# Optimization experiments

Measured on AMD Instinct MI355X. Metric: run time of the kernel, lower is better.

## Reference

```python
import jax, jax.numpy as jnp
import numpy as np

EPS = 1e-5
NUM_HEADS = 8


def setup_inputs() -> dict:
    key = jax.random.key(0)
    ks = jax.random.split(key, 6)
    B, C, S = 4, 512, 2048
    std = 0.02
    return {
        "hidden_states": jax.random.normal(ks[0], (B, C, S), dtype=jnp.float32),
        "gn_weight": jnp.ones((C,), dtype=jnp.float32),
        "gn_bias": jnp.zeros((C,), dtype=jnp.float32),
        "wq": jax.random.normal(ks[1], (C, C), dtype=jnp.float32) * std,
        "bq": jnp.zeros((C,), dtype=jnp.float32),
        "wk": jax.random.normal(ks[2], (C, C), dtype=jnp.float32) * std,
        "bk": jnp.zeros((C,), dtype=jnp.float32),
        "wv": jax.random.normal(ks[3], (C, C), dtype=jnp.float32) * std,
        "bv": jnp.zeros((C,), dtype=jnp.float32),
        "wo": jax.random.normal(ks[4], (C, C), dtype=jnp.float32) * std,
        "bo": jnp.zeros((C,), dtype=jnp.float32),
    }


def reference(hidden_states, gn_weight, gn_bias, wq, bq, wk, bk, wv, bv, wo, bo):
    # hidden_states: [B, C, S]
    x = hidden_states
    B, C, S = x.shape
    H = NUM_HEADS
    D = C // H

    # GroupNorm with 1 group: normalize over (C, S) per sample
    mean = jnp.mean(x, axis=(1, 2), keepdims=True)
    var = jnp.var(x, axis=(1, 2), keepdims=True)
    h = (x - mean) * jax.lax.rsqrt(var + EPS)
    h = h * gn_weight[None, :, None] + gn_bias[None, :, None]

    h = jnp.swapaxes(h, 1, 2)  # [B, S, C]

    q = h @ wq.T + bq  # [B, S, C]
    k = h @ wk.T + bk
    v = h @ wv.T + bv

    # split heads: [B, H, S, D]
    q = q.reshape(B, S, H, D).transpose(0, 2, 1, 3)
    k = k.reshape(B, S, H, D).transpose(0, 2, 1, 3)
    v = v.reshape(B, S, H, D).transpose(0, 2, 1, 3)

    scale = 1.0 / (D ** 0.25)  # applied to both q and k, as in source
    scores = jnp.einsum('bhqd,bhkd->bhqk', q * scale, k * scale)
    probs = jax.nn.softmax(scores, axis=-1)
    out = jnp.einsum('bhqk,bhkd->bhqd', probs, v)  # [B, H, S, D]

    out = out.transpose(0, 2, 1, 3).reshape(B, S, C)  # [B, S, C]
    out = out @ wo.T + bo
    out = jnp.swapaxes(out, 1, 2)  # [B, C, S]
    return out + hidden_states
```

## Files before the change

kernel.cpp:

```cpp
#include <hip/hip_runtime.h>

typedef __attribute__((ext_vector_type(8))) __bf16 bf16x8;
typedef __attribute__((ext_vector_type(4))) __bf16 bf16x4;
typedef __attribute__((ext_vector_type(4))) float f32x4;
typedef __attribute__((ext_vector_type(16))) float f32x16;

#define BSZ 4
#define CCH 512
#define SEQ 2048
#define NH  8
#define HD  64

__device__ __forceinline__ f32x4 mfma16(bf16x8 a, bf16x8 b, f32x4 c) {
  return __builtin_amdgcn_mfma_f32_16x16x32_bf16(a, b, c, 0, 0, 0);
}
__device__ __forceinline__ f32x16 mfma32(bf16x8 a, bf16x8 b, f32x16 c) {
  return __builtin_amdgcn_mfma_f32_32x32x16_bf16(a, b, c, 0, 0, 0);
}

__device__ __forceinline__ void gload16(const void* g, void* l) {
  __builtin_amdgcn_global_load_lds((const __attribute__((address_space(1))) void*)g,
                                   (__attribute__((address_space(3))) void*)l,
                                   16, 0, 0);
}

__device__ __forceinline__ unsigned cvtpk(float lo, float hi) {
  unsigned r;
  asm("v_cvt_pk_bf16_f32 %0, %1, %2" : "=v"(r) : "v"(lo), "v"(hi));
  return r;
}
__device__ __forceinline__ void pl32swap(unsigned& a, unsigned& b) {
  asm("v_permlane32_swap_b32 %0, %1" : "+v"(a), "+v"(b));
}

#define WAIT_VM(N)                                          \
  asm volatile("s_waitcnt vmcnt(" #N ")" ::: "memory");     \
  __builtin_amdgcn_sched_barrier(0);                        \
  __builtin_amdgcn_s_barrier();

__global__ __launch_bounds__(256) void gn_partial(const float* __restrict__ x,
                                                  float* __restrict__ stats) {
  int b = blockIdx.y;
  const float4* xb = (const float4*)(x + ((size_t)b << 20) + (size_t)blockIdx.x * 16384);
  int tid = threadIdx.x;
  float s = 0.f, sq = 0.f;
#pragma unroll
  for (int i = 0; i < 16; ++i) {
    float4 v = xb[i * 256 + tid];
    s  += v.x + v.y + v.z + v.w;
    sq += v.x * v.x + v.y * v.y + v.z * v.z + v.w * v.w;
  }
#pragma unroll
  for (int o = 32; o > 0; o >>= 1) { s += __shfl_down(s, o); sq += __shfl_down(sq, o); }
  __shared__ float ls[4], lq[4];
  int w = tid >> 6;
  if ((tid & 63) == 0) { ls[w] = s; lq[w] = sq; }
  __syncthreads();
  if (tid == 0) {
    float S = ls[0] + ls[1] + ls[2] + ls[3];
    float Q = lq[0] + lq[1] + lq[2] + lq[3];
    atomicAdd(&stats[b], S);
    atomicAdd(&stats[4 + b], Q);
  }
}

__global__ void gn_final(float* stats) {
  int t = threadIdx.x;
  if (t < 4) {
    const float n = 1048576.f;
    float mean = stats[t] / n;
    float var = stats[4 + t] / n - mean * mean;
    stats[8 + t]  = mean;
    stats[12 + t] = rsqrtf(var + 1e-5f);
  }
}

__global__ __launch_bounds__(256) void norm_tr(const float* __restrict__ x,
                                               const float* __restrict__ gw,
                                               const float* __restrict__ gb,
                                               const float* __restrict__ stats,
                                               __bf16* __restrict__ h) {
  int s0 = blockIdx.x * 64, c0 = blockIdx.y * 64, b = blockIdx.z;
  float mean = stats[8 + b], rstd = stats[12 + b];
  const float* xb = x + ((size_t)b << 20);
  __shared__ __align__(16) __bf16 tile[64][72];
  int tid = threadIdx.x;
#pragma unroll
  for (int j = 0; j < 16; ++j) {
    int e = tid + j * 256;
    int cl = e >> 6, sl = e & 63;
    float vv = xb[(size_t)(c0 + cl) * 2048 + s0 + sl];
    float hn = (vv - mean) * rstd * gw[c0 + cl] + gb[c0 + cl];
    tile[cl][sl] = (__bf16)hn;
  }
  __syncthreads();
#pragma unroll
  for (int j = 0; j < 2; ++j) {
    int row = (tid >> 3) + j * 32;
    int cg = tid & 7;
    bf16x8 pk;
#pragma unroll
    for (int e = 0; e < 8; ++e) pk[e] = tile[cg * 8 + e][row];
    *(bf16x8*)&h[(size_t)((b << 11) + s0 + row) * 512 + c0 + cg * 8] = pk;
  }
}

__global__ __launch_bounds__(256) void wcvt(const float* __restrict__ wq, const float* __restrict__ wk,
                                            const float* __restrict__ wv, const float* __restrict__ wo,
                                            __bf16* __restrict__ out) {
  int i = blockIdx.x * 256 + threadIdx.x;
  out[i]          = (__bf16)wq[i];
  out[262144 + i] = (__bf16)wk[i];
  out[524288 + i] = (__bf16)wv[i];
  out[786432 + i] = (__bf16)wo[i];
}

__global__ __launch_bounds__(256) void gemm_qkv(const __bf16* __restrict__ A, const __bf16* __restrict__ Wb,
                                                const float* __restrict__ bq, const float* __restrict__ bk,
                                                const float* __restrict__ bvv,
                                                __bf16* __restrict__ oq, __bf16* __restrict__ ok,
                                                __bf16* __restrict__ ovt) {
  __shared__ __align__(16) __bf16 sA[3][4096];
  __shared__ __align__(16) __bf16 sB[3][4096];
  int z = blockIdx.z;
  const __bf16* W = Wb + (size_t)z * 262144;
  const float* bias = z == 0 ? bq : (z == 1 ? bk : bvv);
  int tid = threadIdx.x, wid = tid >> 6, l = tid & 63;
  int m0 = blockIdx.x * 128, n0 = blockIdx.y * 128;
  int wm = (wid >> 1) * 64, wn = (wid & 1) * 64;
  int l16 = l & 15, lg = l >> 4;
  f32x4 zero = {0.f, 0.f, 0.f, 0.f};
  f32x4 acc[4][4];
#pragma unroll
  for (int mt = 0; mt < 4; ++mt)
#pragma unroll
    for (int nt = 0; nt < 4; ++nt) acc[mt][nt] = zero;

  int srow = wid * 32 + (l >> 2);
  int scol = ((l & 3) ^ ((l >> 3) & 3)) * 8;
  int rs = (lg ^ ((l16 >> 1) & 3)) * 8;

  auto STG = [&](int buf, int k0) {
#pragma unroll
    for (int t = 0; t < 2; ++t) {
      gload16(A + (size_t)(m0 + srow + t * 16) * 512 + k0 + scol, &sA[buf][(wid * 32 + t * 16) * 32]);
      gload16(W + (size_t)(n0 + srow + t * 16) * 512 + k0 + scol, &sB[buf][(wid * 32 + t * 16) * 32]);
    }
  };
  auto CMP = [&](int buf) {
    bf16x8 af[4], bfr[4];
#pragma unroll
    for (int mt = 0; mt < 4; ++mt) af[mt] = *(const bf16x8*)&sA[buf][(wm + mt * 16 + l16) * 32 + rs];
#pragma unroll
    for (int nt = 0; nt < 4; ++nt) bfr[nt] = *(const bf16x8*)&sB[buf][(wn + nt * 16 + l16) * 32 + rs];
    __builtin_amdgcn_s_setprio(1);
#pragma unroll
    for (int mt = 0; mt < 4; ++mt)
#pragma unroll
      for (int nt = 0; nt < 4; ++nt) acc[mt][nt] = mfma16(af[mt], bfr[nt], acc[mt][nt]);
    __builtin_amdgcn_s_setprio(0);
  };

  STG(0, 0); STG(1, 32);
  int bc = 0, sb = 2;
  for (int t = 0; t < 15; ++t) {
    WAIT_VM(4);
    if (t < 14) { STG(sb, (t + 2) * 32); sb = sb == 2 ? 0 : sb + 1; }
    CMP(bc); bc = bc == 2 ? 0 : bc + 1;
  }
  WAIT_VM(0);
  CMP(bc);

  if (z < 2) {
    __bf16* out = z == 0 ? oq : ok;
#pragma unroll
    for (int nt = 0; nt < 4; ++nt) {
      int col = n0 + wn + nt * 16 + l16;
      float bb = bias[col];
#pragma unroll
      for (int mt = 0; mt < 4; ++mt)
#pragma unroll
        for (int r = 0; r < 4; ++r)
          out[(size_t)(m0 + wm + mt * 16 + lg * 4 + r) * 512 + col] = (__bf16)(acc[mt][nt][r] + bb);
    }
  } else {
#pragma unroll
    for (int nt = 0; nt < 4; ++nt) {
      int col = n0 + wn + nt * 16 + l16;
      float bb = bias[col];
      int hd = col >> 6, dd = col & 63;
#pragma unroll
      for (int mt = 0; mt < 4; ++mt) {
        int sg = m0 + wm + mt * 16 + lg * 4;
        int bI = sg >> 11, sl = sg & 2047;
        bf16x4 pk;
#pragma unroll
        for (int r = 0; r < 4; ++r) pk[r] = (__bf16)(acc[mt][nt][r] + bb);
        *(bf16x4*)&ovt[((size_t)((bI * 8 + hd) * 64 + dd)) * 2048 + sl] = pk;
      }
    }
  }
}

__global__ __launch_bounds__(256) void attn(const __bf16* __restrict__ q, const __bf16* __restrict__ k,
                                            const __bf16* __restrict__ vt, __bf16* __restrict__ ao) {
  const float C2 = 0.18033688011f;
  const float THR = 8.0f;
  int tid = threadIdx.x, w = tid >> 6, l = tid & 63;
  int q0w = blockIdx.x * 128 + w * 32;
  int hh = blockIdx.y, b = blockIdx.z;
  int l31 = l & 31, hi = l >> 5;

  __shared__ __align__(16) __bf16 smem[3][8192];

  bf16x8 qf[4];
  {
    const __bf16* qrow = q + ((size_t)((b << 11) + q0w + l31)) * 512 + hh * 64 + hi * 8;
#pragma unroll
    for (int dt = 0; dt < 4; ++dt) qf[dt] = *(const bf16x8*)&qrow[dt * 16];
  }

  const __bf16* kbase = k + ((size_t)(b << 11)) * 512 + hh * 64;
  const __bf16* vtb = vt + ((size_t)((b * 8 + hh) * 64)) * 2048;

  f32x16 zero16 = {};
  f32x16 o2[2];
  o2[0] = zero16; o2[1] = zero16;
  float m_run = -3.0e38f, l_run = 0.f;

  int rloc = l >> 3;
  int slotg = (l & 7) ^ rloc;
  int swz = (l31 & 7);

  auto STAGE = [&](int buf, int kv0) {
#pragma unroll
    for (int i = 0; i < 4; ++i) {
      int c = w * 4 + i;
      int row = (c & 7) * 8 + rloc;
      if (c < 8) {
        gload16(kbase + (size_t)(kv0 + row) * 512 + slotg * 8, &smem[buf][c * 512]);
      } else {
        gload16(vtb + (size_t)row * 2048 + kv0 + slotg * 8, &smem[buf][4096 + (c - 8) * 512]);
      }
    }
  };

  auto COMPUTE = [&](int buf) {
    const __bf16* Kt = &smem[buf][0];
    const __bf16* Vts = &smem[buf][4096];
    f32x16 sc[2];
#pragma unroll
    for (int kb = 0; kb < 2; ++kb) {
      sc[kb] = zero16;
      int r = kb * 32 + l31;
      __builtin_amdgcn_s_setprio(1);
#pragma unroll
      for (int dt = 0; dt < 4; ++dt) {
        bf16x8 kf = *(const bf16x8*)&Kt[r * 64 + ((dt * 2 + hi) ^ swz) * 8];
        sc[kb] = mfma32(kf, qf[dt], sc[kb]);
      }
      __builtin_amdgcn_s_setprio(0);
    }

    float mx01 = -3.0e38f;
#pragma unroll
    for (int kb = 0; kb < 2; ++kb)
#pragma unroll
      for (int r = 0; r < 16; ++r) mx01 = fmaxf(mx01, sc[kb][r]);
    mx01 = fmaxf(mx01, __shfl_xor(mx01, 32));
    mx01 *= C2;
    if (!__all(mx01 <= m_run + THR)) {
      float mnew = fmaxf(m_run, mx01);
      float alpha = exp2f(m_run - mnew);
      m_run = mnew;
      l_run *= alpha;
#pragma unroll
      for (int dblk = 0; dblk < 2; ++dblk)
#pragma unroll
        for (int r = 0; r < 16; ++r) o2[dblk][r] *= alpha;
    }
    float rsum = 0.f;
#pragma unroll
    for (int kb = 0; kb < 2; ++kb)
#pragma unroll
      for (int r = 0; r < 16; ++r) {
        float p = exp2f(__builtin_fmaf(sc[kb][r], C2, -m_run));
        rsum += p;
        sc[kb][r] = p;
      }
    rsum += __shfl_xor(rsum, 32);
    l_run += rsum;

#pragma unroll
    for (int t = 0; t < 4; ++t) {
      int kb = t >> 1, h8 = (t & 1) * 8;
      unsigned u0 = cvtpk(sc[kb][h8 + 0], sc[kb][h8 + 1]);
      unsigned u1 = cvtpk(sc[kb][h8 + 2], sc[kb][h8 + 3]);
      unsigned u2 = cvtpk(sc[kb][h8 + 4], sc[kb][h8 + 5]);
      unsigned u3 = cvtpk(sc[kb][h8 + 6], sc[kb][h8 + 7]);
      pl32swap(u0, u2);
      pl32swap(u1, u3);
      union { unsigned u[4]; bf16x8 v; } pb;
      pb.u[0] = u0; pb.u[1] = u1; pb.u[2] = u2; pb.u[3] = u3;
      __builtin_amdgcn_s_setprio(1);
#pragma unroll
      for (int dblk = 0; dblk < 2; ++dblk) {
        int r = dblk * 32 + l31;
        bf16x8 vf = *(const bf16x8*)&Vts[r * 64 + ((t * 2 + hi) ^ swz) * 8];
        o2[dblk] = mfma32(vf, pb.v, o2[dblk]);
      }
      __builtin_amdgcn_s_setprio(0);
    }
  };

  STAGE(0, 0);
  STAGE(1, 64);
  int bc = 0, sb = 2;
  for (int t = 0; t < 31; ++t) {
    WAIT_VM(4);
    if (t < 30) { STAGE(sb, (t + 2) * 64); sb = sb == 2 ? 0 : sb + 1; }
    COMPUTE(bc); bc = bc == 2 ? 0 : bc + 1;
  }
  WAIT_VM(0);
  COMPUTE(bc);

  float invl = 1.0f / l_run;
  __bf16* T = &smem[0][w * 2048];
  int swzq = (l31 & 7) * 8;
#pragma unroll
  for (int dblk = 0; dblk < 2; ++dblk)
#pragma unroll
    for (int g = 0; g < 4; ++g) {
      unsigned w0 = cvtpk(o2[dblk][g * 4 + 0] * invl, o2[dblk][g * 4 + 1] * invl);
      unsigned w1 = cvtpk(o2[dblk][g * 4 + 2] * invl, o2[dblk][g * 4 + 3] * invl);
      int d4 = dblk * 32 + g * 8 + hi * 4;
      uint2 pk2; pk2.x = w0; pk2.y = w1;
      *(uint2*)&T[l31 * 64 + (d4 ^ swzq)] = pk2;
    }
  int qr = l >> 1, hf = l & 1;
  int swzr = (qr & 7) * 8;
  __bf16* aorow = ao + (size_t)((b << 11) + q0w + qr) * 512 + hh * 64;
#pragma unroll
  for (int m = 0; m < 2; ++m) {
    int e = hf * 32 + m * 16;
    bf16x8 v0 = *(const bf16x8*)&T[qr * 64 + ((e) ^ swzr)];
    bf16x8 v1 = *(const bf16x8*)&T[qr * 64 + ((e + 8) ^ swzr)];
    *(bf16x8*)&aorow[e] = v0;
    *(bf16x8*)&aorow[e + 8] = v1;
  }
}

__global__ __launch_bounds__(256) void gemm_proj(const __bf16* __restrict__ A, const __bf16* __restrict__ W,
                                                 const float* __restrict__ bias,
                                                 const float* __restrict__ resid,
                                                 float* __restrict__ outp) {
  __shared__ __align__(16) union UU {
    struct SS { __bf16 a[3][4096]; __bf16 b[3][4096]; } s;
    float st[128 * 129];
  } u;
  int tid = threadIdx.x, wid = tid >> 6, l = tid & 63;
  int m0 = blockIdx.x * 128, n0 = blockIdx.y * 128;
  int wm = (wid >> 1) * 64, wn = (wid & 1) * 64;
  int l16 = l & 15, lg = l >> 4;
  f32x4 zero = {0.f, 0.f, 0.f, 0.f};
  f32x4 acc[4][4];
#pragma unroll
  for (int mt = 0; mt < 4; ++mt)
#pragma unroll
    for (int nt = 0; nt < 4; ++nt) acc[mt][nt] = zero;

  int srow = wid * 32 + (l >> 2);
  int scol = ((l & 3) ^ ((l >> 3) & 3)) * 8;
  int rs = (lg ^ ((l16 >> 1) & 3)) * 8;

  auto STG = [&](int buf, int k0) {
#pragma unroll
    for (int t = 0; t < 2; ++t) {
      gload16(A + (size_t)(m0 + srow + t * 16) * 512 + k0 + scol, &u.s.a[buf][(wid * 32 + t * 16) * 32]);
      gload16(W + (size_t)(n0 + srow + t * 16) * 512 + k0 + scol, &u.s.b[buf][(wid * 32 + t * 16) * 32]);
    }
  };
  auto CMP = [&](int buf) {
    bf16x8 af[4], bfr[4];
#pragma unroll
    for (int mt = 0; mt < 4; ++mt) af[mt] = *(const bf16x8*)&u.s.a[buf][(wm + mt * 16 + l16) * 32 + rs];
#pragma unroll
    for (int nt = 0; nt < 4; ++nt) bfr[nt] = *(const bf16x8*)&u.s.b[buf][(wn + nt * 16 + l16) * 32 + rs];
    __builtin_amdgcn_s_setprio(1);
#pragma unroll
    for (int mt = 0; mt < 4; ++mt)
#pragma unroll
      for (int nt = 0; nt < 4; ++nt) acc[mt][nt] = mfma16(af[mt], bfr[nt], acc[mt][nt]);
    __builtin_amdgcn_s_setprio(0);
  };

  STG(0, 0); STG(1, 32);
  int bc = 0, sb = 2;
  for (int t = 0; t < 15; ++t) {
    WAIT_VM(4);
    if (t < 14) { STG(sb, (t + 2) * 32); sb = sb == 2 ? 0 : sb + 1; }
    CMP(bc); bc = bc == 2 ? 0 : bc + 1;
  }
  WAIT_VM(0);
  CMP(bc);

  __syncthreads();
#pragma unroll
  for (int nt = 0; nt < 4; ++nt) {
    int col = wn + nt * 16 + l16;
    float bb = bias[n0 + col];
#pragma unroll
    for (int mt = 0; mt < 4; ++mt)
#pragma unroll
      for (int r = 0; r < 4; ++r)
        u.st[(wm + mt * 16 + lg * 4 + r) * 129 + col] = acc[mt][nt][r] + bb;
  }
  __syncthreads();
  int b = m0 >> 11;
  int sbase = m0 & 2047;
  const float* rb = resid + ((size_t)b << 20);
  float* ob = outp + ((size_t)b << 20);
#pragma unroll
  for (int it = 0; it < 16; ++it) {
    int c = (tid >> 5) + it * 8;
    int s4 = (tid & 31) * 4;
    float4 r4 = *(const float4*)&rb[(size_t)(n0 + c) * 2048 + sbase + s4];
    float4 o4;
    o4.x = u.st[(s4 + 0) * 129 + c] + r4.x;
    o4.y = u.st[(s4 + 1) * 129 + c] + r4.y;
    o4.z = u.st[(s4 + 2) * 129 + c] + r4.z;
    o4.w = u.st[(s4 + 3) * 129 + c] + r4.w;
    *(float4*)&ob[(size_t)(n0 + c) * 2048 + sbase + s4] = o4;
  }
}

extern "C" void kernel_launch(void* const* d_in, const int* in_sizes, int n_in,
                              void* d_out, int out_size, void* d_ws, size_t ws_size,
                              hipStream_t stream) {
  const float* x   = (const float*)d_in[0];
  const float* gw  = (const float*)d_in[1];
  const float* gb  = (const float*)d_in[2];
  const float* wqf = (const float*)d_in[3];
  const float* bqf = (const float*)d_in[4];
  const float* wkf = (const float*)d_in[5];
  const float* bkf = (const float*)d_in[6];
  const float* wvf = (const float*)d_in[7];
  const float* bvf = (const float*)d_in[8];
  const float* wof = (const float*)d_in[9];
  const float* bof = (const float*)d_in[10];
  float* outp = (float*)d_out;

  char* ws = (char*)d_ws;
  float* stats = (float*)ws;
  const size_t MAT = (size_t)8192 * 512;
  __bf16* h  = (__bf16*)(ws + 256);
  __bf16* q  = h + MAT;
  __bf16* k  = q + MAT;
  __bf16* vt = k + MAT;
  __bf16* ao = vt + MAT;
  __bf16* wB = ao + MAT;

  hipMemsetAsync(stats, 0, 256, stream);
  gn_partial<<<dim3(64, 4), 256, 0, stream>>>(x, stats);
  gn_final<<<1, 64, 0, stream>>>(stats);
  norm_tr<<<dim3(32, 8, 4), 256, 0, stream>>>(x, gw, gb, stats, h);
  wcvt<<<1024, 256, 0, stream>>>(wqf, wkf, wvf, wof, wB);
  gemm_qkv<<<dim3(64, 4, 3), 256, 0, stream>>>(h, wB, bqf, bkf, bvf, q, k, vt);
  attn<<<dim3(16, 8, 4), 256, 0, stream>>>(q, k, vt, ao);
  gemm_proj<<<dim3(64, 4), 256, 0, stream>>>(ao, wB + 3 * 262144, bof, x, outp);
}
```

Before: 208.2 us.

## Drop stats memset and finalize kernel, stage V-transpose store, MFMA row-sum

GroupNorm partial sums are now written to per-block slots and reduced inside norm_tr, which removes the memset, the atomics and the gn_final launch. The V^T epilogue of the QKV GEMM is staged through LDS so it can issue coalesced 16-byte stores. In attention, the softmax denominator is accumulated with an extra MFMA against a vector of ones instead of a scalar sum plus shuffle, and the K/V LDS swizzle gains an extra XOR term to reduce bank conflicts. Each norm_tr block now re-reads 128 stats values, and the ones-MFMA adds matrix-core work and sums bf16-rounded probabilities.

```diff
diff --git a/kernel.cpp b/kernel.cpp
--- a/kernel.cpp
+++ b/kernel.cpp
@@ -57,21 +57,8 @@
   if ((tid & 63) == 0) { ls[w] = s; lq[w] = sq; }
   __syncthreads();
   if (tid == 0) {
-    float S = ls[0] + ls[1] + ls[2] + ls[3];
-    float Q = lq[0] + lq[1] + lq[2] + lq[3];
-    atomicAdd(&stats[b], S);
-    atomicAdd(&stats[4 + b], Q);
-  }
-}
-
-__global__ void gn_final(float* stats) {
-  int t = threadIdx.x;
-  if (t < 4) {
-    const float n = 1048576.f;
-    float mean = stats[t] / n;
-    float var = stats[4 + t] / n - mean * mean;
-    stats[8 + t]  = mean;
-    stats[12 + t] = rsqrtf(var + 1e-5f);
+    stats[b * 64 + blockIdx.x]       = ls[0] + ls[1] + ls[2] + ls[3];
+    stats[256 + b * 64 + blockIdx.x] = lq[0] + lq[1] + lq[2] + lq[3];
   }
 }
 
@@ -81,7 +68,14 @@
                                                const float* __restrict__ stats,
                                                __bf16* __restrict__ h) {
   int s0 = blockIdx.x * 64, c0 = blockIdx.y * 64, b = blockIdx.z;
-  float mean = stats[8 + b], rstd = stats[12 + b];
+  float sacc = 0.f, qacc = 0.f;
+  for (int i = 0; i < 64; ++i) {
+    sacc += stats[b * 64 + i];
+    qacc += stats[256 + b * 64 + i];
+  }
+  const float inv_n = 1.0f / 1048576.f;
+  float mean = sacc * inv_n;
+  float rstd = rsqrtf(qacc * inv_n - mean * mean + 1e-5f);
   const float* xb = x + ((size_t)b << 20);
   __shared__ __align__(16) __bf16 tile[64][72];
   int tid = threadIdx.x;
@@ -120,8 +114,10 @@
                                                 const float* __restrict__ bvv,
                                                 __bf16* __restrict__ oq, __bf16* __restrict__ ok,
                                                 __bf16* __restrict__ ovt) {
-  __shared__ __align__(16) __bf16 sA[3][4096];
-  __shared__ __align__(16) __bf16 sB[3][4096];
+  __shared__ __align__(16) union QU {
+    struct SS { __bf16 a[3][4096]; __bf16 b[3][4096]; } s;
+    __bf16 t[128 * 136];
+  } u;
   int z = blockIdx.z;
   const __bf16* W = Wb + (size_t)z * 262144;
   const float* bias = z == 0 ? bq : (z == 1 ? bk : bvv);
@@ -143,16 +139,16 @@
   auto STG = [&](int buf, int k0) {
 #pragma unroll
     for (int t = 0; t < 2; ++t) {
-      gload16(A + (size_t)(m0 + srow + t * 16) * 512 + k0 + scol, &sA[buf][(wid * 32 + t * 16) * 32]);
-      gload16(W + (size_t)(n0 + srow + t * 16) * 512 + k0 + scol, &sB[buf][(wid * 32 + t * 16) * 32]);
+      gload16(A + (size_t)(m0 + srow + t * 16) * 512 + k0 + scol, &u.s.a[buf][(wid * 32 + t * 16) * 32]);
+      gload16(W + (size_t)(n0 + srow + t * 16) * 512 + k0 + scol, &u.s.b[buf][(wid * 32 + t * 16) * 32]);
     }
   };
   auto CMP = [&](int buf) {
     bf16x8 af[4], bfr[4];
 #pragma unroll
-    for (int mt = 0; mt < 4; ++mt) af[mt] = *(const bf16x8*)&sA[buf][(wm + mt * 16 + l16) * 32 + rs];
-#pragma unroll
-    for (int nt = 0; nt < 4; ++nt) bfr[nt] = *(const bf16x8*)&sB[buf][(wn + nt * 16 + l16) * 32 + rs];
+    for (int mt = 0; mt < 4; ++mt) af[mt] = *(const bf16x8*)&u.s.a[buf][(wm + mt * 16 + l16) * 32 + rs];
+#pragma unroll
+    for (int nt = 0; nt < 4; ++nt) bfr[nt] = *(const bf16x8*)&u.s.b[buf][(wn + nt * 16 + l16) * 32 + rs];
     __builtin_amdgcn_s_setprio(1);
 #pragma unroll
     for (int mt = 0; mt < 4; ++mt)
@@ -184,20 +180,27 @@
           out[(size_t)(m0 + wm + mt * 16 + lg * 4 + r) * 512 + col] = (__bf16)(acc[mt][nt][r] + bb);
     }
   } else {
+    __syncthreads();
 #pragma unroll
     for (int nt = 0; nt < 4; ++nt) {
-      int col = n0 + wn + nt * 16 + l16;
-      float bb = bias[col];
-      int hd = col >> 6, dd = col & 63;
-#pragma unroll
-      for (int mt = 0; mt < 4; ++mt) {
-        int sg = m0 + wm + mt * 16 + lg * 4;
-        int bI = sg >> 11, sl = sg & 2047;
-        bf16x4 pk;
-#pragma unroll
-        for (int r = 0; r < 4; ++r) pk[r] = (__bf16)(acc[mt][nt][r] + bb);
-        *(bf16x4*)&ovt[((size_t)((bI * 8 + hd) * 64 + dd)) * 2048 + sl] = pk;
-      }
+      int col = wn + nt * 16 + l16;
+      float bb = bias[n0 + col];
+#pragma unroll
+      for (int mt = 0; mt < 4; ++mt)
+#pragma unroll
+        for (int r = 0; r < 4; ++r)
+          u.t[col * 136 + wm + mt * 16 + lg * 4 + r] = (__bf16)(acc[mt][nt][r] + bb);
+    }
+    __syncthreads();
+    int bI = m0 >> 11, sbase = m0 & 2047;
+#pragma unroll
+    for (int p = 0; p < 8; ++p) {
+      int row = (tid >> 4) + p * 16;
+      int ck = tid & 15;
+      bf16x8 v = *(const bf16x8*)&u.t[row * 136 + ck * 8];
+      int colg = n0 + row;
+      int hd = colg >> 6, dd = colg & 63;
+      *(bf16x8*)&ovt[((size_t)((bI * 8 + hd) * 64 + dd)) * 2048 + sbase + ck * 8] = v;
     }
   }
 }
@@ -219,6 +222,9 @@
 #pragma unroll
     for (int dt = 0; dt < 4; ++dt) qf[dt] = *(const bf16x8*)&qrow[dt * 16];
   }
+  bf16x8 ones;
+#pragma unroll
+  for (int j = 0; j < 8; ++j) ones[j] = (__bf16)1.0f;
 
   const __bf16* kbase = k + ((size_t)(b << 11)) * 512 + hh * 64;
   const __bf16* vtb = vt + ((size_t)((b * 8 + hh) * 64)) * 2048;
@@ -226,21 +232,24 @@
   f32x16 zero16 = {};
   f32x16 o2[2];
   o2[0] = zero16; o2[1] = zero16;
-  float m_run = -3.0e38f, l_run = 0.f;
+  f32x16 facc = zero16;
+  float m_run = -3.0e38f;
 
   int rloc = l >> 3;
-  int slotg = (l & 7) ^ rloc;
   int swz = (l31 & 7);
+  int q3 = (l31 >> 3) & 3;
 
   auto STAGE = [&](int buf, int kv0) {
 #pragma unroll
     for (int i = 0; i < 4; ++i) {
       int c = w * 4 + i;
-      int row = (c & 7) * 8 + rloc;
+      int cc = c & 7;
+      int row = cc * 8 + rloc;
+      int sg = (((l & 7) ^ rloc ^ (cc & 3))) * 8;
       if (c < 8) {
-        gload16(kbase + (size_t)(kv0 + row) * 512 + slotg * 8, &smem[buf][c * 512]);
+        gload16(kbase + (size_t)(kv0 + row) * 512 + sg, &smem[buf][c * 512]);
       } else {
-        gload16(vtb + (size_t)row * 2048 + kv0 + slotg * 8, &smem[buf][4096 + (c - 8) * 512]);
+        gload16(vtb + (size_t)row * 2048 + kv0 + sg, &smem[buf][4096 + cc * 512]);
       }
     }
   };
@@ -256,7 +265,7 @@
       __builtin_amdgcn_s_setprio(1);
 #pragma unroll
       for (int dt = 0; dt < 4; ++dt) {
-        bf16x8 kf = *(const bf16x8*)&Kt[r * 64 + ((dt * 2 + hi) ^ swz) * 8];
+        bf16x8 kf = *(const bf16x8*)&Kt[r * 64 + ((dt * 2 + hi) ^ swz ^ q3) * 8];
         sc[kb] = mfma32(kf, qf[dt], sc[kb]);
       }
       __builtin_amdgcn_s_setprio(0);
@@ -273,23 +282,18 @@
       float mnew = fmaxf(m_run, mx01);
       float alpha = exp2f(m_run - mnew);
       m_run = mnew;
-      l_run *= alpha;
+#pragma unroll
+      for (int r = 0; r < 16; ++r) facc[r] *= alpha;
 #pragma unroll
       for (int dblk = 0; dblk < 2; ++dblk)
 #pragma unroll
         for (int r = 0; r < 16; ++r) o2[dblk][r] *= alpha;
     }
-    float rsum = 0.f;
 #pragma unroll
     for (int kb = 0; kb < 2; ++kb)
 #pragma unroll
-      for (int r = 0; r < 16; ++r) {
-        float p = exp2f(__builtin_fmaf(sc[kb][r], C2, -m_run));
-        rsum += p;
-        sc[kb][r] = p;
-      }
-    rsum += __shfl_xor(rsum, 32);
-    l_run += rsum;
+      for (int r = 0; r < 16; ++r)
+        sc[kb][r] = exp2f(__builtin_fmaf(sc[kb][r], C2, -m_run));
 
 #pragma unroll
     for (int t = 0; t < 4; ++t) {
@@ -303,10 +307,11 @@
       union { unsigned u[4]; bf16x8 v; } pb;
       pb.u[0] = u0; pb.u[1] = u1; pb.u[2] = u2; pb.u[3] = u3;
       __builtin_amdgcn_s_setprio(1);
+      facc = mfma32(ones, pb.v, facc);
 #pragma unroll
       for (int dblk = 0; dblk < 2; ++dblk) {
         int r = dblk * 32 + l31;
-        bf16x8 vf = *(const bf16x8*)&Vts[r * 64 + ((t * 2 + hi) ^ swz) * 8];
+        bf16x8 vf = *(const bf16x8*)&Vts[r * 64 + ((t * 2 + hi) ^ swz ^ q3) * 8];
         o2[dblk] = mfma32(vf, pb.v, o2[dblk]);
       }
       __builtin_amdgcn_s_setprio(0);
@@ -324,7 +329,7 @@
   WAIT_VM(0);
   COMPUTE(bc);
 
-  float invl = 1.0f / l_run;
+  float invl = 1.0f / facc[0];
   __bf16* T = &smem[0][w * 2048];
   int swzq = (l31 & 7) * 8;
 #pragma unroll
@@ -453,16 +458,14 @@
   char* ws = (char*)d_ws;
   float* stats = (float*)ws;
   const size_t MAT = (size_t)8192 * 512;
-  __bf16* h  = (__bf16*)(ws + 256);
+  __bf16* h  = (__bf16*)(ws + 4096);
   __bf16* q  = h + MAT;
   __bf16* k  = q + MAT;
   __bf16* vt = k + MAT;
   __bf16* ao = vt + MAT;
   __bf16* wB = ao + MAT;
 
-  hipMemsetAsync(stats, 0, 256, stream);
   gn_partial<<<dim3(64, 4), 256, 0, stream>>>(x, stats);
-  gn_final<<<1, 64, 0, stream>>>(stats);
   norm_tr<<<dim3(32, 8, 4), 256, 0, stream>>>(x, gw, gb, stats, h);
   wcvt<<<1024, 256, 0, stream>>>(wqf, wkf, wvf, wof, wB);
   gemm_qkv<<<dim3(64, 4, 3), 256, 0, stream>>>(h, wB, bqf, bkf, bvf, q, k, vt);
```

New measurement: 190.3 us. -8.6%, faster.
